# Optimization experiments

Measured on AMD Instinct MI355X. Metric: run time of the kernel, lower is better.

## Reference

```python
import jax, jax.numpy as jnp
import numpy as np

TEMPERATURE = 0.5
HEAD_DIM = 64
NUM_HEADS = 4

N_NODES = 50000
N_EDGES = 800000
DIM = 256


def setup_inputs() -> dict:
    key = jax.random.key(0)
    ks = jax.random.split(key, 7)
    h = jax.random.normal(ks[0], (N_NODES, DIM), dtype=jnp.float32)
    src = jax.random.randint(ks[1], (N_EDGES,), 0, N_NODES)
    dst = jax.random.randint(ks[2], (N_EDGES,), 0, N_NODES)
    attn_q = jax.random.normal(ks[3], (DIM, NUM_HEADS * HEAD_DIM), dtype=jnp.float32) * 0.02
    attn_k = jax.random.normal(ks[4], (DIM, NUM_HEADS * HEAD_DIM), dtype=jnp.float32) * 0.02
    W = jax.random.normal(ks[5], (DIM, DIM), dtype=jnp.float32) * (1.0 / np.sqrt(DIM))
    b = jnp.zeros((DIM,), dtype=jnp.float32)
    return {"h": h, "src": src, "dst": dst, "attn_q": attn_q, "attn_k": attn_k, "W": W, "b": b}


def _edge_softmax_by_dst(a, dst, n_nodes):
    # softmax over incoming edges of each destination node (DGL edge_softmax)
    m = jax.ops.segment_max(a, dst, num_segments=n_nodes)
    e = jnp.exp(a - m[dst])
    s = jax.ops.segment_sum(e, dst, num_segments=n_nodes)
    return e / s[dst]


def reference(h, src, dst, attn_q, attn_k, W, b):
    n = h.shape[0]
    v = h @ W.T + b                         # iv Linear: [N, D]
    q = h @ attn_q                          # [N, H*64]
    k = h @ attn_k                          # [N, H*64]
    # per-edge score: mean over heads then over head_dim == mean over all H*64,
    # preceded by /8 -> dot(q_src, k_dst) / (8 * H * 64)
    scale = 1.0 / (8.0 * NUM_HEADS * HEAD_DIM)
    a = jnp.einsum('ed,ed->e', q[src], k[dst]) * scale   # [E]
    # global standardization over all edges (std unbiased=False)
    m = a.mean()
    s = jnp.sqrt(((a - m) ** 2).mean())
    a = (a - m) / s / TEMPERATURE
    a = _edge_softmax_by_dst(a, dst, n)     # [E]
    # message passing: sum_{e: dst(e)=i} a_e * v[src(e)]
    out = jax.ops.segment_sum(v[src] * a[:, None], dst, num_segments=n)  # [N, D]
    return out, a
```

## Files before the change

kernel.cpp:

```cpp
#include <hip/hip_runtime.h>
#include <math.h>

#define DIM 256
#define NQKV 768
#define STAT_BLOCKS 2048

typedef float  f32x4 __attribute__((ext_vector_type(4)));
typedef short  bs8   __attribute__((ext_vector_type(8)));

__device__ __forceinline__ ushort f2bf(float f) {
    unsigned int u = __float_as_uint(f);
    u += 0x7fffu + ((u >> 16) & 1u);
    return (ushort)(u >> 16);
}
__device__ __forceinline__ float bf2f(ushort u) {
    return __uint_as_float(((unsigned int)u) << 16);
}

#define MFMA16(c, a, b) \
    asm("s_nop 1\n\tv_mfma_f32_16x16x32_bf16 %0, %1, %2, %0" : "+v"(c) : "v"(a), "v"(b))

__global__ __launch_bounds__(256) void conv_h(
    const float* __restrict__ h, ushort* __restrict__ h_bf, int total8)
{
    const int idx = blockIdx.x * 256 + threadIdx.x;
    if (idx >= total8) return;
    const float4* hp = (const float4*)(h + (size_t)idx * 8);
    float4 a = hp[0], b = hp[1];
    uint4 o;
    o.x = (unsigned)f2bf(a.x) | ((unsigned)f2bf(a.y) << 16);
    o.y = (unsigned)f2bf(a.z) | ((unsigned)f2bf(a.w) << 16);
    o.z = (unsigned)f2bf(b.x) | ((unsigned)f2bf(b.y) << 16);
    o.w = (unsigned)f2bf(b.z) | ((unsigned)f2bf(b.w) << 16);
    *(uint4*)(h_bf + (size_t)idx * 8) = o;
}

__global__ __launch_bounds__(256) void build_bt(
    const float* __restrict__ attn_q, const float* __restrict__ attn_k,
    const float* __restrict__ W, ushort* __restrict__ bt)
{
    const int n = blockIdx.x;
    const int k = threadIdx.x;
    float val;
    if (n < 256)      val = attn_q[(size_t)k * 256 + n];
    else if (n < 512) val = attn_k[(size_t)k * 256 + (n - 256)];
    else              val = W[(size_t)(n - 512) * 256 + k];
    bt[(size_t)n * 256 + k] = f2bf(val);
}

__global__ __launch_bounds__(256) void gemm_qkv_mfma(
    const ushort* __restrict__ h_bf, const ushort* __restrict__ bt,
    const float* __restrict__ bias, ushort* __restrict__ qkv, int M)
{
    __shared__ __align__(16) ushort As[128 * 40];
    __shared__ __align__(16) ushort Bs[128 * 40];

    const int bm = blockIdx.x * 128;
    const int bn = blockIdx.y * 128;
    const int t    = threadIdx.x;
    const int lane = t & 63;
    const int wid  = t >> 6;
    const int wm   = wid >> 1;
    const int wn   = wid & 1;
    const int fr   = lane & 15;
    const int ko   = (lane >> 4) * 8;

    f32x4 acc[4][4];
    #pragma unroll
    for (int i = 0; i < 4; ++i)
        #pragma unroll
        for (int j = 0; j < 4; ++j)
            acc[i][j] = (f32x4){0.f, 0.f, 0.f, 0.f};

    for (int k0 = 0; k0 < DIM; k0 += 32) {
        #pragma unroll
        for (int ii = 0; ii < 2; ++ii) {
            const int s   = t * 2 + ii;
            const int row = s >> 2;
            const int sl  = s & 3;
            int ga = bm + row; if (ga > M - 1) ga = M - 1;
            uint4 va = *(const uint4*)(h_bf + (size_t)ga * 256 + k0 + sl * 8);
            *(uint4*)(As + row * 40 + sl * 8) = va;
            uint4 vb = *(const uint4*)(bt + (size_t)(bn + row) * 256 + k0 + sl * 8);
            *(uint4*)(Bs + row * 40 + sl * 8) = vb;
        }
        __syncthreads();

        bs8 af[4], bf_[4];
        #pragma unroll
        for (int f = 0; f < 4; ++f) {
            af[f]  = *(const bs8*)(As + (wm * 64 + f * 16 + fr) * 40 + ko);
            bf_[f] = *(const bs8*)(Bs + (wn * 64 + f * 16 + fr) * 40 + ko);
        }
        #pragma unroll
        for (int fm = 0; fm < 4; ++fm)
            #pragma unroll
            for (int fn = 0; fn < 4; ++fn)
                MFMA16(acc[fm][fn], af[fm], bf_[fn]);

        __syncthreads();
    }

    asm volatile("s_nop 7\n\ts_nop 7\n\ts_nop 7" ::: );

    #pragma unroll
    for (int fm = 0; fm < 4; ++fm) {
        const int rowbase = bm + wm * 64 + fm * 16 + (lane >> 4) * 4;
        #pragma unroll
        for (int fn = 0; fn < 4; ++fn) {
            const int col = bn + wn * 64 + fn * 16 + fr;
            float bv = (col >= 512) ? bias[col - 512] : 0.f;
            #pragma unroll
            for (int r = 0; r < 4; ++r) {
                const int row = rowbase + r;
                if (row < M)
                    qkv[(size_t)row * NQKV + col] = f2bf(acc[fm][fn][r] + bv);
            }
        }
    }
}

__global__ __launch_bounds__(256) void edge_dot(
    const ushort* __restrict__ qkv,
    const int* __restrict__ src, const int* __restrict__ dst,
    float* __restrict__ a_raw, int* __restrict__ deg,
    double* __restrict__ partials, int E)
{
    const int wid  = threadIdx.x >> 6;
    const int lane = threadIdx.x & 63;
    const int nwaves = gridDim.x * 4;

    double lsum = 0.0, lsum2 = 0.0;
    for (int e = blockIdx.x * 4 + wid; e < E; e += nwaves) {
        const int s = src[e];
        const int d = dst[e];
        ushort4 qa = *(const ushort4*)(qkv + (size_t)s * NQKV + lane * 4);
        ushort4 kb = *(const ushort4*)(qkv + (size_t)d * NQKV + 256 + lane * 4);
        float dotv = bf2f(qa.x) * bf2f(kb.x) + bf2f(qa.y) * bf2f(kb.y)
                   + bf2f(qa.z) * bf2f(kb.z) + bf2f(qa.w) * bf2f(kb.w);
        #pragma unroll
        for (int off = 32; off; off >>= 1) dotv += __shfl_xor(dotv, off);
        if (lane == 0) {
            a_raw[e] = dotv;
            atomicAdd(&deg[d], 1);
            lsum  += (double)dotv;
            lsum2 += (double)dotv * (double)dotv;
        }
    }

    __shared__ double bsum[4], bsum2[4];
    if (lane == 0) { bsum[wid] = lsum; bsum2[wid] = lsum2; }
    __syncthreads();
    if (threadIdx.x == 0) {
        partials[blockIdx.x]             = bsum[0] + bsum[1] + bsum[2] + bsum[3];
        partials[gridDim.x + blockIdx.x] = bsum2[0] + bsum2[1] + bsum2[2] + bsum2[3];
    }
}

__global__ __launch_bounds__(1024) void scan_rowptr(
    const int* __restrict__ deg, int* __restrict__ row_ptr, int N,
    const double* __restrict__ partials, float* __restrict__ coef, int E)
{
    const int tid  = threadIdx.x;
    const int lane = tid & 63;
    const int wv   = tid >> 6;

    __shared__ double red[1024];
    double s1 = 0.0, s2 = 0.0;
    for (int i = tid; i < STAT_BLOCKS; i += 1024) {
        s1 += partials[i];
        s2 += partials[STAT_BLOCKS + i];
    }
    red[tid] = s1;
    __syncthreads();
    for (int off = 512; off; off >>= 1) {
        if (tid < off) red[tid] += red[tid + off];
        __syncthreads();
    }
    const double tot1 = red[0];
    __syncthreads();
    red[tid] = s2;
    __syncthreads();
    for (int off = 512; off; off >>= 1) {
        if (tid < off) red[tid] += red[tid + off];
        __syncthreads();
    }
    const double tot2 = red[0];
    __syncthreads();

    if (tid == 0) {
        const double mean = tot1 / (double)E;
        const double var  = tot2 / (double)E - mean * mean;
        coef[0] = (float)mean;
        coef[1] = (float)(1.0 / (sqrt(var) * 0.5));
        row_ptr[0] = 0;
    }

    __shared__ int woff[17];
    __shared__ int carryS;
    if (tid == 0) carryS = 0;
    __syncthreads();

    for (int base = 0; base < N; base += 4096) {
        int x[4], pre[4];
        int run = 0;
        #pragma unroll
        for (int j = 0; j < 4; ++j) {
            const int i = base + tid * 4 + j;
            const int v = (i < N) ? deg[i] : 0;
            pre[j] = run; x[j] = v; run += v;
        }
        int incl = run;
        #pragma unroll
        for (int off = 1; off < 64; off <<= 1) {
            int y = __shfl_up(incl, off);
            if (lane >= off) incl += y;
        }
        const int wex = incl - run;
        if (lane == 63) woff[wv] = incl;
        __syncthreads();
        if (wv == 0) {
            int wtot = (lane < 16) ? woff[lane] : 0;
            int winc = wtot;
            #pragma unroll
            for (int off = 1; off < 16; off <<= 1) {
                int y = __shfl_up(winc, off);
                if (lane >= off) winc += y;
            }
            if (lane < 16) woff[lane] = winc - wtot;
            if (lane == 15) woff[16] = winc;
        }
        __syncthreads();
        const int basev = carryS + woff[wv] + wex;
        #pragma unroll
        for (int j = 0; j < 4; ++j) {
            const int i = base + tid * 4 + j;
            if (i < N) row_ptr[i + 1] = basev + pre[j] + x[j];
        }
        __syncthreads();
        if (tid == 0) carryS += woff[16];
        __syncthreads();
    }
}

__global__ __launch_bounds__(256) void scatter_edges(
    const int* __restrict__ dst, const int* __restrict__ row_ptr,
    int* __restrict__ cursor, int* __restrict__ edge_idx, int E)
{
    const int e = blockIdx.x * 256 + threadIdx.x;
    if (e < E) {
        const int d = dst[e];
        const int pos = atomicAdd(&cursor[d], 1);
        edge_idx[row_ptr[d] + pos] = e;
    }
}

__global__ __launch_bounds__(256) void edge_softmax(
    const float* __restrict__ a_raw, const int* __restrict__ row_ptr,
    const int* __restrict__ edge_idx, const float* __restrict__ coef,
    float* __restrict__ a_out, int N)
{
    const int wid  = threadIdx.x >> 6;
    const int lane = threadIdx.x & 63;
    const int node = blockIdx.x * 4 + wid;
    if (node >= N) return;

    const int s  = row_ptr[node];
    const int en = row_ptr[node + 1];
    const float mean = coef[0];
    const float mul  = coef[1];

    float mx = -INFINITY;
    for (int j = s + lane; j < en; j += 64)
        mx = fmaxf(mx, (a_raw[edge_idx[j]] - mean) * mul);
    #pragma unroll
    for (int off = 32; off; off >>= 1) mx = fmaxf(mx, __shfl_xor(mx, off));

    float sum = 0.f;
    for (int j = s + lane; j < en; j += 64)
        sum += __expf((a_raw[edge_idx[j]] - mean) * mul - mx);
    #pragma unroll
    for (int off = 32; off; off >>= 1) sum += __shfl_xor(sum, off);

    const float rcp = 1.0f / sum;
    for (int j = s + lane; j < en; j += 64) {
        const int e = edge_idx[j];
        a_out[e] = __expf((a_raw[e] - mean) * mul - mx) * rcp;
    }
}

__global__ __launch_bounds__(256) void aggregate(
    const ushort* __restrict__ qkv, const float* __restrict__ a_out,
    const int* __restrict__ src, const int* __restrict__ row_ptr,
    const int* __restrict__ edge_idx, float* __restrict__ out, int N)
{
    const int node = blockIdx.x;
    const int col  = threadIdx.x;
    const int s  = row_ptr[node];
    const int en = row_ptr[node + 1];

    __shared__ float ae[64];
    __shared__ int   asrc[64];

    float acc = 0.f;
    for (int base = s; base < en; base += 64) {
        const int cnt = min(64, en - base);
        if (threadIdx.x < cnt) {
            const int e = edge_idx[base + threadIdx.x];
            ae[threadIdx.x]   = a_out[e];
            asrc[threadIdx.x] = src[e];
        }
        __syncthreads();
        for (int j = 0; j < cnt; ++j)
            acc += ae[j] * bf2f(qkv[(size_t)asrc[j] * NQKV + 512 + col]);
        __syncthreads();
    }
    out[(size_t)node * DIM + col] = acc;
}

extern "C" void kernel_launch(void* const* d_in, const int* in_sizes, int n_in,
                              void* d_out, int out_size, void* d_ws, size_t ws_size,
                              hipStream_t stream)
{
    const float* h      = (const float*)d_in[0];
    const int*   src    = (const int*)d_in[1];
    const int*   dst    = (const int*)d_in[2];
    const float* attn_q = (const float*)d_in[3];
    const float* attn_k = (const float*)d_in[4];
    const float* W      = (const float*)d_in[5];
    const float* bias   = (const float*)d_in[6];

    const int N = in_sizes[0] / DIM;
    const int E = in_sizes[1];

    float* out   = (float*)d_out;
    float* a_out = out + (size_t)N * DIM;

    char* ws = (char*)d_ws;
    ushort* h_bf  = (ushort*)ws; ws += (size_t)N * DIM * 2;
    ushort* qkv   = (ushort*)ws; ws += (size_t)N * NQKV * 2;
    ushort* bt    = (ushort*)ws; ws += (size_t)NQKV * DIM * 2;
    float* a_raw  = (float*)ws;  ws += (size_t)E * 4;
    int* edge_idx = (int*)ws;    ws += (size_t)E * 4;
    int* deg      = (int*)ws;    ws += (size_t)N * 4;
    int* cursor   = (int*)ws;    ws += (size_t)N * 4;
    double* partials = (double*)ws; ws += (size_t)STAT_BLOCKS * 2 * 8;
    float* coef   = (float*)ws;  ws += 8;
    int* row_ptr  = (int*)ws;    ws += (size_t)(N + 1) * 4;

    hipMemsetAsync(deg,    0, (size_t)N * 4, stream);
    hipMemsetAsync(cursor, 0, (size_t)N * 4, stream);

    const int total8 = N * DIM / 8;
    conv_h<<<(total8 + 255) / 256, 256, 0, stream>>>(h, h_bf, total8);
    build_bt<<<NQKV, 256, 0, stream>>>(attn_q, attn_k, W, bt);

    dim3 gg((N + 127) / 128, NQKV / 128);
    gemm_qkv_mfma<<<gg, 256, 0, stream>>>(h_bf, bt, bias, qkv, N);

    edge_dot<<<STAT_BLOCKS, 256, 0, stream>>>(qkv, src, dst, a_raw, deg, partials, E);
    scan_rowptr<<<1, 1024, 0, stream>>>(deg, row_ptr, N, partials, coef, E);
    scatter_edges<<<(E + 255) / 256, 256, 0, stream>>>(dst, row_ptr, cursor, edge_idx, E);
    edge_softmax<<<(N + 3) / 4, 256, 0, stream>>>(a_raw, row_ptr, edge_idx, coef, a_out, N);
    aggregate<<<N, 256, 0, stream>>>(qkv, a_out, src, row_ptr, edge_idx, out, N);
}
```

Measured before the change: 508.7 us.

## Build CSR first, compute edge scores in CSR order, fuse softmax into aggregation

The CSR structure is now built from dst before any scoring. The scatter step writes packed (src, dst, edge id) records in destination-sorted order, reusing the bf16 h buffer's workspace. Edge dot products are then computed over these contiguous records, so k rows of the same destination are reused and scores are stored CSR-ordered. The separate softmax kernel is removed: aggregation computes the per-node exp sum, the normalized weights and the a_out scatter inline. The max-subtraction pass is dropped, which relies on the standardized scores staying small enough not to overflow exp.

```diff
diff --git a/kernel.cpp b/kernel.cpp
--- a/kernel.cpp
+++ b/kernel.cpp
@@ -120,81 +120,21 @@
     }
 }
 
-__global__ __launch_bounds__(256) void edge_dot(
-    const ushort* __restrict__ qkv,
-    const int* __restrict__ src, const int* __restrict__ dst,
-    float* __restrict__ a_raw, int* __restrict__ deg,
-    double* __restrict__ partials, int E)
-{
-    const int wid  = threadIdx.x >> 6;
-    const int lane = threadIdx.x & 63;
-    const int nwaves = gridDim.x * 4;
-
-    double lsum = 0.0, lsum2 = 0.0;
-    for (int e = blockIdx.x * 4 + wid; e < E; e += nwaves) {
-        const int s = src[e];
-        const int d = dst[e];
-        ushort4 qa = *(const ushort4*)(qkv + (size_t)s * NQKV + lane * 4);
-        ushort4 kb = *(const ushort4*)(qkv + (size_t)d * NQKV + 256 + lane * 4);
-        float dotv = bf2f(qa.x) * bf2f(kb.x) + bf2f(qa.y) * bf2f(kb.y)
-                   + bf2f(qa.z) * bf2f(kb.z) + bf2f(qa.w) * bf2f(kb.w);
-        #pragma unroll
-        for (int off = 32; off; off >>= 1) dotv += __shfl_xor(dotv, off);
-        if (lane == 0) {
-            a_raw[e] = dotv;
-            atomicAdd(&deg[d], 1);
-            lsum  += (double)dotv;
-            lsum2 += (double)dotv * (double)dotv;
-        }
-    }
-
-    __shared__ double bsum[4], bsum2[4];
-    if (lane == 0) { bsum[wid] = lsum; bsum2[wid] = lsum2; }
-    __syncthreads();
-    if (threadIdx.x == 0) {
-        partials[blockIdx.x]             = bsum[0] + bsum[1] + bsum[2] + bsum[3];
-        partials[gridDim.x + blockIdx.x] = bsum2[0] + bsum2[1] + bsum2[2] + bsum2[3];
-    }
+__global__ __launch_bounds__(256) void deg_count(
+    const int* __restrict__ dst, int* __restrict__ deg, int E)
+{
+    const int e = blockIdx.x * 256 + threadIdx.x;
+    if (e < E) atomicAdd(&deg[dst[e]], 1);
 }
 
 __global__ __launch_bounds__(1024) void scan_rowptr(
-    const int* __restrict__ deg, int* __restrict__ row_ptr, int N,
-    const double* __restrict__ partials, float* __restrict__ coef, int E)
+    const int* __restrict__ deg, int* __restrict__ row_ptr, int N)
 {
     const int tid  = threadIdx.x;
     const int lane = tid & 63;
     const int wv   = tid >> 6;
 
-    __shared__ double red[1024];
-    double s1 = 0.0, s2 = 0.0;
-    for (int i = tid; i < STAT_BLOCKS; i += 1024) {
-        s1 += partials[i];
-        s2 += partials[STAT_BLOCKS + i];
-    }
-    red[tid] = s1;
-    __syncthreads();
-    for (int off = 512; off; off >>= 1) {
-        if (tid < off) red[tid] += red[tid + off];
-        __syncthreads();
-    }
-    const double tot1 = red[0];
-    __syncthreads();
-    red[tid] = s2;
-    __syncthreads();
-    for (int off = 512; off; off >>= 1) {
-        if (tid < off) red[tid] += red[tid + off];
-        __syncthreads();
-    }
-    const double tot2 = red[0];
-    __syncthreads();
-
-    if (tid == 0) {
-        const double mean = tot1 / (double)E;
-        const double var  = tot2 / (double)E - mean * mean;
-        coef[0] = (float)mean;
-        coef[1] = (float)(1.0 / (sqrt(var) * 0.5));
-        row_ptr[0] = 0;
-    }
+    if (tid == 0) row_ptr[0] = 0;
 
     __shared__ int woff[17];
     __shared__ int carryS;
@@ -244,78 +184,155 @@
 }
 
 __global__ __launch_bounds__(256) void scatter_edges(
-    const int* __restrict__ dst, const int* __restrict__ row_ptr,
-    int* __restrict__ cursor, int* __restrict__ edge_idx, int E)
+    const int* __restrict__ src, const int* __restrict__ dst,
+    const int* __restrict__ row_ptr, int* __restrict__ cursor,
+    int4* __restrict__ edata, int E)
 {
     const int e = blockIdx.x * 256 + threadIdx.x;
     if (e < E) {
         const int d = dst[e];
-        const int pos = atomicAdd(&cursor[d], 1);
-        edge_idx[row_ptr[d] + pos] = e;
-    }
-}
-
-__global__ __launch_bounds__(256) void edge_softmax(
-    const float* __restrict__ a_raw, const int* __restrict__ row_ptr,
-    const int* __restrict__ edge_idx, const float* __restrict__ coef,
-    float* __restrict__ a_out, int N)
-{
+        const int pos = row_ptr[d] + atomicAdd(&cursor[d], 1);
+        edata[pos] = make_int4(src[e], d, e, 0);
+    }
+}
+
+__global__ __launch_bounds__(256) void edge_dot_csr(
+    const ushort* __restrict__ qkv, const int4* __restrict__ edata,
+    float* __restrict__ a_rawc, double* __restrict__ partials, int E)
+{
+    const int lane = threadIdx.x & 63;
     const int wid  = threadIdx.x >> 6;
-    const int lane = threadIdx.x & 63;
-    const int node = blockIdx.x * 4 + wid;
-    if (node >= N) return;
-
+    const int w    = blockIdx.x * 4 + wid;
+    const int nw   = gridDim.x * 4;
+    const int chunk = (E + nw - 1) / nw;
+    const int p0 = w * chunk;
+    const int p1 = min(E, p0 + chunk);
+
+    double lsum = 0.0, lsum2 = 0.0;
+    int p = p0;
+    for (; p + 2 <= p1; p += 2) {
+        const int4 e0 = edata[p];
+        const int4 e1 = edata[p + 1];
+        ushort4 qa0 = *(const ushort4*)(qkv + (size_t)e0.x * NQKV + lane * 4);
+        ushort4 kb0 = *(const ushort4*)(qkv + (size_t)e0.y * NQKV + 256 + lane * 4);
+        ushort4 qa1 = *(const ushort4*)(qkv + (size_t)e1.x * NQKV + lane * 4);
+        ushort4 kb1 = *(const ushort4*)(qkv + (size_t)e1.y * NQKV + 256 + lane * 4);
+        float d0 = bf2f(qa0.x) * bf2f(kb0.x) + bf2f(qa0.y) * bf2f(kb0.y)
+                 + bf2f(qa0.z) * bf2f(kb0.z) + bf2f(qa0.w) * bf2f(kb0.w);
+        float d1 = bf2f(qa1.x) * bf2f(kb1.x) + bf2f(qa1.y) * bf2f(kb1.y)
+                 + bf2f(qa1.z) * bf2f(kb1.z) + bf2f(qa1.w) * bf2f(kb1.w);
+        #pragma unroll
+        for (int off = 32; off; off >>= 1) {
+            d0 += __shfl_xor(d0, off);
+            d1 += __shfl_xor(d1, off);
+        }
+        if (lane == 0) {
+            a_rawc[p]     = d0;
+            a_rawc[p + 1] = d1;
+            lsum  += (double)d0 + (double)d1;
+            lsum2 += (double)d0 * (double)d0 + (double)d1 * (double)d1;
+        }
+    }
+    if (p < p1) {
+        const int4 e0 = edata[p];
+        ushort4 qa0 = *(const ushort4*)(qkv + (size_t)e0.x * NQKV + lane * 4);
+        ushort4 kb0 = *(const ushort4*)(qkv + (size_t)e0.y * NQKV + 256 + lane * 4);
+        float d0 = bf2f(qa0.x) * bf2f(kb0.x) + bf2f(qa0.y) * bf2f(kb0.y)
+                 + bf2f(qa0.z) * bf2f(kb0.z) + bf2f(qa0.w) * bf2f(kb0.w);
+        #pragma unroll
+        for (int off = 32; off; off >>= 1) d0 += __shfl_xor(d0, off);
+        if (lane == 0) {
+            a_rawc[p] = d0;
+            lsum  += (double)d0;
+            lsum2 += (double)d0 * (double)d0;
+        }
+    }
+
+    __shared__ double bsum[4], bsum2[4];
+    if (lane == 0) { bsum[wid] = lsum; bsum2[wid] = lsum2; }
+    __syncthreads();
+    if (threadIdx.x == 0) {
+        partials[blockIdx.x]             = bsum[0] + bsum[1] + bsum[2] + bsum[3];
+        partials[gridDim.x + blockIdx.x] = bsum2[0] + bsum2[1] + bsum2[2] + bsum2[3];
+    }
+}
+
+__global__ __launch_bounds__(256) void finalize_coef(
+    const double* __restrict__ partials, float* __restrict__ coef, int E)
+{
+    __shared__ double red[256];
+    const int tid = threadIdx.x;
+    double s1 = 0.0, s2 = 0.0;
+    for (int i = tid; i < STAT_BLOCKS; i += 256) {
+        s1 += partials[i];
+        s2 += partials[STAT_BLOCKS + i];
+    }
+    red[tid] = s1;
+    __syncthreads();
+    for (int off = 128; off; off >>= 1) {
+        if (tid < off) red[tid] += red[tid + off];
+        __syncthreads();
+    }
+    const double tot1 = red[0];
+    __syncthreads();
+    red[tid] = s2;
+    __syncthreads();
+    for (int off = 128; off; off >>= 1) {
+        if (tid < off) red[tid] += red[tid + off];
+        __syncthreads();
+    }
+    if (tid == 0) {
+        const double mean = tot1 / (double)E;
+        const double var  = red[0] / (double)E - mean * mean;
+        coef[0] = (float)mean;
+        coef[1] = (float)(1.0 / (sqrt(var) * 0.5));
+    }
+}
+
+__global__ __launch_bounds__(256) void agg_fused(
+    const ushort* __restrict__ qkv, const float* __restrict__ a_rawc,
+    const int4* __restrict__ edata, const int* __restrict__ row_ptr,
+    const float* __restrict__ coef,
+    float* __restrict__ out, float* __restrict__ a_out, int N)
+{
+    const int node = blockIdx.x;
+    const int tid  = threadIdx.x;
+    const int lane = tid & 63;
+    const int wv   = tid >> 6;
     const int s  = row_ptr[node];
     const int en = row_ptr[node + 1];
     const float mean = coef[0];
     const float mul  = coef[1];
 
-    float mx = -INFINITY;
-    for (int j = s + lane; j < en; j += 64)
-        mx = fmaxf(mx, (a_raw[edge_idx[j]] - mean) * mul);
+    float lsum = 0.f;
+    for (int j = s + tid; j < en; j += 256)
+        lsum += __expf((a_rawc[j] - mean) * mul);
     #pragma unroll
-    for (int off = 32; off; off >>= 1) mx = fmaxf(mx, __shfl_xor(mx, off));
-
-    float sum = 0.f;
-    for (int j = s + lane; j < en; j += 64)
-        sum += __expf((a_raw[edge_idx[j]] - mean) * mul - mx);
-    #pragma unroll
-    for (int off = 32; off; off >>= 1) sum += __shfl_xor(sum, off);
-
-    const float rcp = 1.0f / sum;
-    for (int j = s + lane; j < en; j += 64) {
-        const int e = edge_idx[j];
-        a_out[e] = __expf((a_raw[e] - mean) * mul - mx) * rcp;
-    }
-}
-
-__global__ __launch_bounds__(256) void aggregate(
-    const ushort* __restrict__ qkv, const float* __restrict__ a_out,
-    const int* __restrict__ src, const int* __restrict__ row_ptr,
-    const int* __restrict__ edge_idx, float* __restrict__ out, int N)
-{
-    const int node = blockIdx.x;
-    const int col  = threadIdx.x;
-    const int s  = row_ptr[node];
-    const int en = row_ptr[node + 1];
+    for (int off = 32; off; off >>= 1) lsum += __shfl_xor(lsum, off);
+    __shared__ float ws4[4];
+    if (lane == 0) ws4[wv] = lsum;
+    __syncthreads();
+    const float rcp = 1.0f / (ws4[0] + ws4[1] + ws4[2] + ws4[3]);
 
     __shared__ float ae[64];
     __shared__ int   asrc[64];
-
     float acc = 0.f;
     for (int base = s; base < en; base += 64) {
         const int cnt = min(64, en - base);
-        if (threadIdx.x < cnt) {
-            const int e = edge_idx[base + threadIdx.x];
-            ae[threadIdx.x]   = a_out[e];
-            asrc[threadIdx.x] = src[e];
-        }
-        __syncthreads();
+        __syncthreads();
+        if (tid < cnt) {
+            const int4 ed = edata[base + tid];
+            const float wgt = __expf((a_rawc[base + tid] - mean) * mul) * rcp;
+            ae[tid]   = wgt;
+            asrc[tid] = ed.x;
+            a_out[ed.z] = wgt;
+        }
+        __syncthreads();
+        #pragma unroll 4
         for (int j = 0; j < cnt; ++j)
-            acc += ae[j] * bf2f(qkv[(size_t)asrc[j] * NQKV + 512 + col]);
-        __syncthreads();
-    }
-    out[(size_t)node * DIM + col] = acc;
+            acc += ae[j] * bf2f(qkv[(size_t)asrc[j] * NQKV + 512 + tid]);
+    }
+    out[(size_t)node * DIM + tid] = acc;
 }
 
 extern "C" void kernel_launch(void* const* d_in, const int* in_sizes, int n_in,
@@ -337,11 +354,12 @@
     float* a_out = out + (size_t)N * DIM;
 
     char* ws = (char*)d_ws;
-    ushort* h_bf  = (ushort*)ws; ws += (size_t)N * DIM * 2;
+    ushort* h_bf  = (ushort*)ws;
+    int4*   edata = (int4*)ws;
+    ws += (size_t)N * DIM * 2;
     ushort* qkv   = (ushort*)ws; ws += (size_t)N * NQKV * 2;
     ushort* bt    = (ushort*)ws; ws += (size_t)NQKV * DIM * 2;
-    float* a_raw  = (float*)ws;  ws += (size_t)E * 4;
-    int* edge_idx = (int*)ws;    ws += (size_t)E * 4;
+    float* a_rawc = (float*)ws;  ws += (size_t)E * 4;
     int* deg      = (int*)ws;    ws += (size_t)N * 4;
     int* cursor   = (int*)ws;    ws += (size_t)N * 4;
     double* partials = (double*)ws; ws += (size_t)STAT_BLOCKS * 2 * 8;
@@ -358,9 +376,10 @@
     dim3 gg((N + 127) / 128, NQKV / 128);
     gemm_qkv_mfma<<<gg, 256, 0, stream>>>(h_bf, bt, bias, qkv, N);
 
-    edge_dot<<<STAT_BLOCKS, 256, 0, stream>>>(qkv, src, dst, a_raw, deg, partials, E);
-    scan_rowptr<<<1, 1024, 0, stream>>>(deg, row_ptr, N, partials, coef, E);
-    scatter_edges<<<(E + 255) / 256, 256, 0, stream>>>(dst, row_ptr, cursor, edge_idx, E);
-    edge_softmax<<<(N + 3) / 4, 256, 0, stream>>>(a_raw, row_ptr, edge_idx, coef, a_out, N);
-    aggregate<<<N, 256, 0, stream>>>(qkv, a_out, src, row_ptr, edge_idx, out, N);
-}
+    deg_count<<<(E + 255) / 256, 256, 0, stream>>>(dst, deg, E);
+    scan_rowptr<<<1, 1024, 0, stream>>>(deg, row_ptr, N);
+    scatter_edges<<<(E + 255) / 256, 256, 0, stream>>>(src, dst, row_ptr, cursor, edata, E);
+    edge_dot_csr<<<STAT_BLOCKS, 256, 0, stream>>>(qkv, edata, a_rawc, partials, E);
+    finalize_coef<<<1, 256, 0, stream>>>(partials, coef, E);
+    agg_fused<<<N, 256, 0, stream>>>(qkv, a_rawc, edata, row_ptr, coef, out, a_out, N);
+}
```

After: 485.4 us. 4.6% less time.
